# Kernel tuning notes

Measured on AMD Instinct MI355X. Metric: run time of the kernel, lower is better.

Reference implementation:

```python
import jax, jax.numpy as jnp
import numpy as np

T, B, I, H, L = 512, 32, 512, 1024, 2


def setup_inputs() -> dict:
    key = jax.random.key(0)
    ks = jax.random.split(key, 10)
    std = 1.0 / np.sqrt(H)
    u = lambda k, shape: jax.random.uniform(k, shape, jnp.float32, -std, std)
    return {
        "x": jax.random.normal(ks[0], (T, B, I), jnp.float32),
        "Wxh0": u(ks[1], (4 * H, I)),
        "bxh0": u(ks[2], (4 * H,)),
        "Whh0": u(ks[3], (4 * H, H)),
        "bhh0": u(ks[4], (4 * H,)),
        "Wxh1": u(ks[5], (4 * H, H)),
        "bxh1": u(ks[6], (4 * H,)),
        "Whh1": u(ks[7], (4 * H, H)),
        "bhh1": u(ks[8], (4 * H,)),
    }


def _lstm_layer(x_seq, Wxh, bxh, Whh, bhh):
    # x_seq: (T, B, D_in). Precompute input projections for all timesteps.
    xg = jnp.einsum('tbi,gi->tbg', x_seq, Wxh) + bxh  # (T, B, 4H)
    h0 = jnp.zeros((x_seq.shape[1], H), x_seq.dtype)
    c0 = jnp.zeros_like(h0)

    def step(carry, xg_t):
        h, c = carry
        gates = xg_t + h @ Whh.T + bhh  # (B, 4H)
        i_g, f_g, g_g, o_g = jnp.split(gates, 4, axis=-1)
        c_new = jax.nn.sigmoid(f_g) * c + jax.nn.sigmoid(i_g) * jnp.tanh(g_g)
        h_new = jax.nn.sigmoid(o_g) * jnp.tanh(c_new)
        return (h_new, c_new), h_new

    (h_T, c_T), hs = jax.lax.scan(step, (h0, c0), xg)
    return hs, h_T, c_T  # hs: (T, B, H)


def reference(x, Wxh0, bxh0, Whh0, bhh0, Wxh1, bxh1, Whh1, bhh1):
    # Layer 0 consumes raw input; layer 1 consumes layer-0 hidden sequence.
    # Processing layer-by-layer is mathematically identical to the original
    # interleaved (t, layer) loop for a stacked unidirectional LSTM.
    hs0, h0T, c0T = _lstm_layer(x, Wxh0, bxh0, Whh0, bhh0)
    hs1, h1T, c1T = _lstm_layer(hs0, Wxh1, bxh1, Whh1, bhh1)
    output = hs1  # (T, B, H): hidden of last layer at each timestep
    h_n = jnp.stack([h0T, h1T])  # (L, B, H)
    c_n = jnp.stack([c0T, c1T])
    return output, h_n, c_n
```

## Files before the change

### kernel.cpp

```cpp
#include <hip/hip_runtime.h>


typedef unsigned short u16;
typedef __attribute__((ext_vector_type(8))) __bf16 bf16x8;
typedef __attribute__((ext_vector_type(8))) u16 u16x8;
typedef __attribute__((ext_vector_type(4))) float f32x4;
typedef __attribute__((ext_vector_type(2))) float f32x2;
typedef __attribute__((ext_vector_type(4))) int i32x4;
typedef __attribute__((ext_vector_type(4))) unsigned int u32x4;

#define HN_OFF 16777216
#define CN_OFF 16842752

__device__ __forceinline__ u16 f2bf(float f) {
  unsigned u = __builtin_bit_cast(unsigned, f);
  u += 0x7FFFu + ((u >> 16) & 1u);
  return (u16)(u >> 16);
}
__device__ __forceinline__ float sgm(float x) { return 1.f / (1.f + __expf(-x)); }
__device__ __forceinline__ float tnh(float x) { return 2.f / (1.f + __expf(-2.f * x)) - 1.f; }

__device__ __forceinline__ bf16x8 ld16(const u16* p) {
  u32x4 v = *reinterpret_cast<const u32x4*>(p);
  return __builtin_bit_cast(bf16x8, v);
}
__device__ __forceinline__ bf16x8 lds16(const char* p) {
  u32x4 v = *reinterpret_cast<const u32x4*>(p);
  return __builtin_bit_cast(bf16x8, v);
}
__device__ __forceinline__ f32x4 mfma16(bf16x8 a, bf16x8 b, f32x4 c) {
  return __builtin_amdgcn_mfma_f32_16x16x32_bf16(a, b, c, 0, 0, 0);
}

__device__ __forceinline__ void poll_flags(const int* f, int lane, int s) {
  const int* p0 = f + (lane << 2);
  const int* p1 = f + 256 + (lane << 2);
  for (;;) {
    i32x4 a, b;
    asm volatile("global_load_dwordx4 %0, %2, off sc0 sc1\n\t"
                 "global_load_dwordx4 %1, %3, off sc0 sc1\n\t"
                 "s_waitcnt vmcnt(0)"
                 : "=v"(a), "=v"(b) : "v"(p0), "v"(p1) : "memory");
    if (__all((a[0] >= s) & (a[1] >= s) & (a[2] >= s) & (a[3] >= s) &
              (b[0] >= s) & (b[1] >= s) & (b[2] >= s) & (b[3] >= s))) break;
  }
}
__device__ __forceinline__ void poll_epoch(const int* ep, int s) {
  for (;;) {
    int e;
    asm volatile("global_load_dword %0, %1, off sc0 sc1\n\ts_waitcnt vmcnt(0)"
                 : "=v"(e) : "v"(ep) : "memory");
    if (e >= s) break;
  }
}

template <int C0, int C1>
__device__ __forceinline__ void chunks_h0(const u16* __restrict__ A,
                                          const char* w0, const char* w1, int lane,
                                          f32x4& p0, f32x4& p1, f32x4& q0, f32x4& q1) {
  const int r = lane & 15, kq = (lane >> 4) * 8, swz = (r & 7) << 4;
#pragma unroll
  for (int c = C0; c < C1; ++c) {
    const u16* ap = A + r * 1024 + c * 32 + kq;
    bf16x8 a0 = ld16(ap);
    bf16x8 a1 = ld16(ap + 16 * 1024);
    bf16x8 b0 = lds16(w0 + r * 3072 + ((c * 64 + kq * 2) ^ swz));
    bf16x8 b1 = lds16(w1 + r * 4096 + (((c + 32) * 64 + kq * 2) ^ swz));
    p0 = mfma16(a0, b0, p0);  p1 = mfma16(a1, b0, p1);
    q0 = mfma16(a0, b1, q0);  q1 = mfma16(a1, b1, q1);
  }
}
template <int C0, int C1>
__device__ __forceinline__ void chunks_h1(const u16* __restrict__ A,
                                          const char* w1, int lane,
                                          f32x4& p0, f32x4& p1) {
  const int r = lane & 15, kq = (lane >> 4) * 8, swz = (r & 7) << 4;
#pragma unroll
  for (int c = C0; c < C1; ++c) {
    const u16* ap = A + r * 1024 + c * 32 + kq;
    bf16x8 a0 = ld16(ap);
    bf16x8 a1 = ld16(ap + 16 * 1024);
    bf16x8 bw = lds16(w1 + r * 4096 + ((c * 64 + kq * 2) ^ swz));
    p0 = mfma16(a0, bw, p0);  p1 = mfma16(a1, bw, p1);
  }
}
template <int C0, int C1>
__device__ __forceinline__ void chunks_x(const u16* __restrict__ A,
                                         const char* w0, int lane,
                                         f32x4& q0, f32x4& q1) {
  const int r = lane & 15, kq = (lane >> 4) * 8, swz = (r & 7) << 4;
#pragma unroll
  for (int c = C0; c < C1; ++c) {
    const u16* ap = A + r * 512 + c * 32 + kq;
    bf16x8 a0 = ld16(ap);
    bf16x8 a1 = ld16(ap + 16 * 512);
    bf16x8 bw = lds16(w0 + r * 3072 + (((c + 32) * 64 + kq * 2) ^ swz));
    q0 = mfma16(a0, bw, q0);  q1 = mfma16(a1, bw, q1);
  }
}

__global__ __launch_bounds__(512, 2) void lstm_fused(
    const u16* __restrict__ xbf,
    const float* __restrict__ Whh0, const float* __restrict__ Wxh0,
    const float* __restrict__ Whh1, const float* __restrict__ Wxh1,
    const float* __restrict__ bxh0, const float* __restrict__ bhh0,
    const float* __restrict__ bxh1, const float* __restrict__ bhh1,
    u16* __restrict__ h0seq, u16* __restrict__ h1seq,
    int* __restrict__ flagbase,
    float* __restrict__ out) {
  extern __shared__ char smem[];
  const char* w0 = smem;
  const char* w1 = smem + 49152;
  auto part = reinterpret_cast<float(*)[32][18]>(smem + 114688);
  float* bias0 = reinterpret_cast<float*>(smem + 151552);
  float* bias1 = reinterpret_cast<float*>(smem + 151616);
  volatile int* go = reinterpret_cast<volatile int*>(smem + 151680);

  int* flag0 = flagbase;
  int* flag1 = flagbase + 256;
  int* epoch = flagbase + 512;

  const int tid = threadIdx.x;
  const int wg = blockIdx.x;
  const int wid = tid >> 6, lane = tid & 63;

  if (tid == 0) go[0] = 0;
  for (int g = tid; g < 3072; g += 512) {
    int n = g / 192, gi = g % 192, kc = gi * 8;
    int gr = ((n >> 2) << 10) + (wg << 2) + (n & 3);
    const float* src = (kc < 1024) ? (Whh0 + gr * 1024 + kc) : (Wxh0 + gr * 512 + (kc - 1024));
    f32x4 lo = *reinterpret_cast<const f32x4*>(src);
    f32x4 hi = *reinterpret_cast<const f32x4*>(src + 4);
    u16x8 o;
    o[0]=f2bf(lo[0]); o[1]=f2bf(lo[1]); o[2]=f2bf(lo[2]); o[3]=f2bf(lo[3]);
    o[4]=f2bf(hi[0]); o[5]=f2bf(hi[1]); o[6]=f2bf(hi[2]); o[7]=f2bf(hi[3]);
    *reinterpret_cast<u16x8*>(smem + n * 3072 + ((gi * 16) ^ ((n & 7) << 4))) = o;
  }
  for (int g = tid; g < 4096; g += 512) {
    int n = g / 256, gi = g % 256, kc = gi * 8;
    int gr = ((n >> 2) << 10) + (wg << 2) + (n & 3);
    const float* src = (kc < 1024) ? (Whh1 + gr * 1024 + kc) : (Wxh1 + gr * 1024 + (kc - 1024));
    f32x4 lo = *reinterpret_cast<const f32x4*>(src);
    f32x4 hi = *reinterpret_cast<const f32x4*>(src + 4);
    u16x8 o;
    o[0]=f2bf(lo[0]); o[1]=f2bf(lo[1]); o[2]=f2bf(lo[2]); o[3]=f2bf(lo[3]);
    o[4]=f2bf(hi[0]); o[5]=f2bf(hi[1]); o[6]=f2bf(hi[2]); o[7]=f2bf(hi[3]);
    *reinterpret_cast<u16x8*>(smem + 49152 + n * 4096 + ((gi * 16) ^ ((n & 7) << 4))) = o;
  }
  if (tid < 16) {
    int gr = ((tid >> 2) << 10) + (wg << 2) + (tid & 3);
    bias0[tid] = bxh0[gr] + bhh0[gr];
    bias1[tid] = bxh1[gr] + bhh1[gr];
  }
  __syncthreads();

  float c0a = 0.f, c0b = 0.f, c1a = 0.f, c1b = 0.f;
  const int bg = lane >> 1, jjb = (lane & 1) << 1;
  const int colb = (wg << 2) + jjb;

  for (int s = 0; s <= 512; ++s) {
    const u16* h0slot = h0seq + s * 32768;
    const u16* h1prev = h1seq + (s - 1) * 32768;
    f32x4 p0 = {0,0,0,0}, p1 = {0,0,0,0}, q0 = {0,0,0,0}, q1 = {0,0,0,0};

    if (wid >= 4 && s < 512) {
      const u16* xbt = xbf + s * 16384;
      if      (wid == 4) chunks_x<0,  4 >(xbt, w0, lane, q0, q1);
      else if (wid == 5) chunks_x<4,  8 >(xbt, w0, lane, q0, q1);
      else if (wid == 6) chunks_x<8,  12>(xbt, w0, lane, q0, q1);
      else               chunks_x<12, 16>(xbt, w0, lane, q0, q1);
    }

    if (s >= 1) {
      if (wid == 0) {
        if (wg == 0) {
          poll_flags(flag0, lane, s);
          if (lane == 0) {
            int sv = s;
            asm volatile("global_store_dword %0, %1, off sc0 sc1"
                         :: "v"(epoch), "v"(sv) : "memory");
          }
        } else {
          poll_epoch(epoch, s);
        }
        if (lane == 0) go[0] = s;
      } else {
        while (go[0] < s) __builtin_amdgcn_s_sleep(1);
      }
    }

    if (wid < 4) {
      if      (wid == 0) chunks_h0<0,  8 >(h0slot, w0, w1, lane, p0, p1, q0, q1);
      else if (wid == 1) chunks_h0<8,  16>(h0slot, w0, w1, lane, p0, p1, q0, q1);
      else if (wid == 2) chunks_h0<16, 24>(h0slot, w0, w1, lane, p0, p1, q0, q1);
      else               chunks_h0<24, 32>(h0slot, w0, w1, lane, p0, p1, q0, q1);
    } else if (s >= 1) {
      if      (wid == 4) chunks_h1<0,  8 >(h1prev, w1, lane, p0, p1);
      else if (wid == 5) chunks_h1<8,  16>(h1prev, w1, lane, p0, p1);
      else if (wid == 6) chunks_h1<16, 24>(h1prev, w1, lane, p0, p1);
      else               chunks_h1<24, 32>(h1prev, w1, lane, p0, p1);
    }

    {
      const int n = lane & 15, br = (lane >> 4) * 4;
#pragma unroll
      for (int j = 0; j < 4; ++j) {
        part[wid][br + j][n]          = p0[j];
        part[wid][br + j + 16][n]     = p1[j];
        part[8 + wid][br + j][n]      = q0[j];
        part[8 + wid][br + j + 16][n] = q1[j];
      }
    }
    __syncthreads();

    if (wid == 1) {
      if (s < 512) {
        float v[4][2];
#pragma unroll
        for (int gi = 0; gi < 4; ++gi) {
          const int n = (gi << 2) + jjb;
          float s0 = bias0[n], s1 = bias0[n + 1];
#pragma unroll
          for (int p = 0; p < 4; ++p) {
            f32x2 a = *reinterpret_cast<const f32x2*>(&part[p][bg][n]);
            f32x2 b = *reinterpret_cast<const f32x2*>(&part[12 + p][bg][n]);
            s0 += a[0] + b[0];  s1 += a[1] + b[1];
          }
          v[gi][0] = s0; v[gi][1] = s1;
        }
        c0a = sgm(v[1][0]) * c0a + sgm(v[0][0]) * tnh(v[2][0]);
        c0b = sgm(v[1][1]) * c0b + sgm(v[0][1]) * tnh(v[2][1]);
        const float ha = sgm(v[3][0]) * tnh(c0a), hb = sgm(v[3][1]) * tnh(c0b);
        unsigned pk = (unsigned)f2bf(ha) | ((unsigned)f2bf(hb) << 16);
        u16* hp = h0seq + (s + 1) * 32768 + bg * 1024 + colb;
        asm volatile("global_store_dword %0, %1, off sc0 sc1" :: "v"(hp), "v"(pk) : "memory");
        asm volatile("s_waitcnt vmcnt(0)" ::: "memory");
        if (lane == 0) {
          int* fp = flag0 + wg;  int fv = s + 1;
          asm volatile("global_store_dword %0, %1, off sc0 sc1" :: "v"(fp), "v"(fv) : "memory");
        }
        if (s == 511) {
          *reinterpret_cast<f32x2*>(out + HN_OFF + bg * 1024 + colb) = f32x2{ha, hb};
          *reinterpret_cast<f32x2*>(out + CN_OFF + bg * 1024 + colb) = f32x2{c0a, c0b};
        }
      }
    } else if (wid == 5) {
      if (s >= 1) {
        float v[4][2];
#pragma unroll
        for (int gi = 0; gi < 4; ++gi) {
          const int n = (gi << 2) + jjb;
          float s0 = bias1[n], s1 = bias1[n + 1];
#pragma unroll
          for (int p = 4; p < 12; ++p) {
            f32x2 a = *reinterpret_cast<const f32x2*>(&part[p][bg][n]);
            s0 += a[0];  s1 += a[1];
          }
          v[gi][0] = s0; v[gi][1] = s1;
        }
        c1a = sgm(v[1][0]) * c1a + sgm(v[0][0]) * tnh(v[2][0]);
        c1b = sgm(v[1][1]) * c1b + sgm(v[0][1]) * tnh(v[2][1]);
        const float ha = sgm(v[3][0]) * tnh(c1a), hb = sgm(v[3][1]) * tnh(c1b);
        unsigned pk = (unsigned)f2bf(ha) | ((unsigned)f2bf(hb) << 16);
        u16* hp = h1seq + s * 32768 + bg * 1024 + colb;
        asm volatile("global_store_dword %0, %1, off sc0 sc1" :: "v"(hp), "v"(pk) : "memory");
        asm volatile("s_waitcnt vmcnt(0)" ::: "memory");
        if (lane == 0) {
          int* fp = flag1 + wg;  int fv = s + 1;
          asm volatile("global_store_dword %0, %1, off sc0 sc1" :: "v"(fp), "v"(fv) : "memory");
        }
        const int t1 = s - 1;
        *reinterpret_cast<f32x2*>(out + t1 * 32768 + bg * 1024 + colb) = f32x2{ha, hb};
        if (t1 == 511) {
          *reinterpret_cast<f32x2*>(out + HN_OFF + 32768 + bg * 1024 + colb) = f32x2{ha, hb};
          *reinterpret_cast<f32x2*>(out + CN_OFF + 32768 + bg * 1024 + colb) = f32x2{c1a, c1b};
        }
      } else if (lane == 0) {
        int* fp = flag1 + wg;  int fv = 1;
        asm volatile("global_store_dword %0, %1, off sc0 sc1" :: "v"(fp), "v"(fv) : "memory");
      }
    }
  }
}

__global__ void cvt_bf16(const float* __restrict__ s, u16* __restrict__ d, int n) {
  int i = (blockIdx.x * blockDim.x + threadIdx.x) * 4;
  const int stride = gridDim.x * blockDim.x * 4;
  typedef __attribute__((ext_vector_type(4))) u16 u16x4;
  for (; i < n; i += stride) {
    f32x4 v = *reinterpret_cast<const f32x4*>(s + i);
    u16x4 o;
    o[0] = f2bf(v[0]); o[1] = f2bf(v[1]); o[2] = f2bf(v[2]); o[3] = f2bf(v[3]);
    *reinterpret_cast<u16x4*>(d + i) = o;
  }
}

extern "C" void kernel_launch(void* const* d_in, const int* in_sizes, int n_in,
                              void* d_out, int out_size, void* d_ws, size_t ws_size,
                              hipStream_t stream) {
  const float* x    = (const float*)d_in[0];
  const float* Wxh0 = (const float*)d_in[1];
  const float* bxh0 = (const float*)d_in[2];
  const float* Whh0 = (const float*)d_in[3];
  const float* bhh0 = (const float*)d_in[4];
  const float* Wxh1 = (const float*)d_in[5];
  const float* bxh1 = (const float*)d_in[6];
  const float* Whh1 = (const float*)d_in[7];
  const float* bhh1 = (const float*)d_in[8];
  char* ws = (char*)d_ws;
  u16* xbf      = (u16*)(ws);
  u16* h0seq    = (u16*)(ws + 16777216);
  u16* h1seq    = (u16*)(ws + 50397184);
  int* flagbase = (int*)(ws + 84017152);

  cvt_bf16<<<2048, 256, 0, stream>>>(x, xbf, 512 * 32 * 512);
  (void)hipMemsetAsync(h0seq, 0, 65536, stream);
  (void)hipMemsetAsync(h1seq, 0, 65536, stream);
  (void)hipMemsetAsync(flagbase, 0, 4096, stream);

  (void)hipFuncSetAttribute(reinterpret_cast<const void*>(lstm_fused),
                            hipFuncAttributeMaxDynamicSharedMemorySize, 151744);
  lstm_fused<<<dim3(256), dim3(512), 151744, stream>>>(
      xbf, Whh0, Wxh0, Whh1, Wxh1, bxh0, bhh0, bxh1, bhh1,
      h0seq, h1seq, flagbase, (float*)d_out);
}
```

Before: 3.517 ms.

## Poll per-block flags directly in every workgroup and batch A-operand loads

Removes the two-hop barrier in which block 0 polled all flags and then published an epoch that the other blocks polled. Every workgroup now polls the flag array itself, cutting one global round-trip of latency from each timestep. The matmul chunk helpers also issue all global A-operand loads before the MFMA loop so their latencies overlap. This raises register pressure and puts more polling traffic on the shared flag lines.

```diff
diff --git a/kernel.cpp b/kernel.cpp
--- a/kernel.cpp
+++ b/kernel.cpp
@@ -45,29 +45,27 @@
               (b[0] >= s) & (b[1] >= s) & (b[2] >= s) & (b[3] >= s))) break;
   }
 }
-__device__ __forceinline__ void poll_epoch(const int* ep, int s) {
-  for (;;) {
-    int e;
-    asm volatile("global_load_dword %0, %1, off sc0 sc1\n\ts_waitcnt vmcnt(0)"
-                 : "=v"(e) : "v"(ep) : "memory");
-    if (e >= s) break;
-  }
-}
 
 template <int C0, int C1>
 __device__ __forceinline__ void chunks_h0(const u16* __restrict__ A,
                                           const char* w0, const char* w1, int lane,
                                           f32x4& p0, f32x4& p1, f32x4& q0, f32x4& q1) {
   const int r = lane & 15, kq = (lane >> 4) * 8, swz = (r & 7) << 4;
-#pragma unroll
-  for (int c = C0; c < C1; ++c) {
-    const u16* ap = A + r * 1024 + c * 32 + kq;
-    bf16x8 a0 = ld16(ap);
-    bf16x8 a1 = ld16(ap + 16 * 1024);
+  constexpr int N = C1 - C0;
+  bf16x8 A0[N], A1[N];
+#pragma unroll
+  for (int i = 0; i < N; ++i) {
+    const u16* ap = A + r * 1024 + (C0 + i) * 32 + kq;
+    A0[i] = ld16(ap);
+    A1[i] = ld16(ap + 16 * 1024);
+  }
+#pragma unroll
+  for (int i = 0; i < N; ++i) {
+    const int c = C0 + i;
     bf16x8 b0 = lds16(w0 + r * 3072 + ((c * 64 + kq * 2) ^ swz));
     bf16x8 b1 = lds16(w1 + r * 4096 + (((c + 32) * 64 + kq * 2) ^ swz));
-    p0 = mfma16(a0, b0, p0);  p1 = mfma16(a1, b0, p1);
-    q0 = mfma16(a0, b1, q0);  q1 = mfma16(a1, b1, q1);
+    p0 = mfma16(A0[i], b0, p0);  p1 = mfma16(A1[i], b0, p1);
+    q0 = mfma16(A0[i], b1, q0);  q1 = mfma16(A1[i], b1, q1);
   }
 }
 template <int C0, int C1>
@@ -75,13 +73,19 @@
                                           const char* w1, int lane,
                                           f32x4& p0, f32x4& p1) {
   const int r = lane & 15, kq = (lane >> 4) * 8, swz = (r & 7) << 4;
-#pragma unroll
-  for (int c = C0; c < C1; ++c) {
-    const u16* ap = A + r * 1024 + c * 32 + kq;
-    bf16x8 a0 = ld16(ap);
-    bf16x8 a1 = ld16(ap + 16 * 1024);
+  constexpr int N = C1 - C0;
+  bf16x8 A0[N], A1[N];
+#pragma unroll
+  for (int i = 0; i < N; ++i) {
+    const u16* ap = A + r * 1024 + (C0 + i) * 32 + kq;
+    A0[i] = ld16(ap);
+    A1[i] = ld16(ap + 16 * 1024);
+  }
+#pragma unroll
+  for (int i = 0; i < N; ++i) {
+    const int c = C0 + i;
     bf16x8 bw = lds16(w1 + r * 4096 + ((c * 64 + kq * 2) ^ swz));
-    p0 = mfma16(a0, bw, p0);  p1 = mfma16(a1, bw, p1);
+    p0 = mfma16(A0[i], bw, p0);  p1 = mfma16(A1[i], bw, p1);
   }
 }
 template <int C0, int C1>
@@ -89,13 +93,19 @@
                                          const char* w0, int lane,
                                          f32x4& q0, f32x4& q1) {
   const int r = lane & 15, kq = (lane >> 4) * 8, swz = (r & 7) << 4;
-#pragma unroll
-  for (int c = C0; c < C1; ++c) {
-    const u16* ap = A + r * 512 + c * 32 + kq;
-    bf16x8 a0 = ld16(ap);
-    bf16x8 a1 = ld16(ap + 16 * 512);
+  constexpr int N = C1 - C0;
+  bf16x8 A0[N], A1[N];
+#pragma unroll
+  for (int i = 0; i < N; ++i) {
+    const u16* ap = A + r * 512 + (C0 + i) * 32 + kq;
+    A0[i] = ld16(ap);
+    A1[i] = ld16(ap + 16 * 512);
+  }
+#pragma unroll
+  for (int i = 0; i < N; ++i) {
+    const int c = C0 + i;
     bf16x8 bw = lds16(w0 + r * 3072 + (((c + 32) * 64 + kq * 2) ^ swz));
-    q0 = mfma16(a0, bw, q0);  q1 = mfma16(a1, bw, q1);
+    q0 = mfma16(A0[i], bw, q0);  q1 = mfma16(A1[i], bw, q1);
   }
 }
 
@@ -118,7 +128,6 @@
 
   int* flag0 = flagbase;
   int* flag1 = flagbase + 256;
-  int* epoch = flagbase + 512;
 
   const int tid = threadIdx.x;
   const int wg = blockIdx.x;
@@ -173,16 +182,7 @@
 
     if (s >= 1) {
       if (wid == 0) {
-        if (wg == 0) {
-          poll_flags(flag0, lane, s);
-          if (lane == 0) {
-            int sv = s;
-            asm volatile("global_store_dword %0, %1, off sc0 sc1"
-                         :: "v"(epoch), "v"(sv) : "memory");
-          }
-        } else {
-          poll_epoch(epoch, s);
-        }
+        poll_flags(flagbase, lane, s);
         if (lane == 0) go[0] = s;
       } else {
         while (go[0] < s) __builtin_amdgcn_s_sleep(1);
@@ -316,7 +316,7 @@
   cvt_bf16<<<2048, 256, 0, stream>>>(x, xbf, 512 * 32 * 512);
   (void)hipMemsetAsync(h0seq, 0, 65536, stream);
   (void)hipMemsetAsync(h1seq, 0, 65536, stream);
-  (void)hipMemsetAsync(flagbase, 0, 4096, stream);
+  (void)hipMemsetAsync(flagbase, 0, 2048, stream);
 
   (void)hipFuncSetAttribute(reinterpret_cast<const void*>(lstm_fused),
                             hipFuncAttributeMaxDynamicSharedMemorySize, 151744);
```

After: 5.691 ms. +61.8%, slower.

## Replace centralized epoch barrier with replicated flags and sentinel-polled hidden loads

Applied to the files above, without the earlier changes.

Removes the two-level barrier (block 0 polls all flags, then broadcasts an epoch) and replaces it with flag arrays replicated eight times. Each block polls its own replica, and producers write the flag without first waiting for their data stores to complete. Hidden-state buffers are pre-filled with a 0xFF sentinel so consumers spin on the actual h data until it is valid, which tolerates flags arriving before data. The weight LDS layout also changes from a swizzled layout to a fragment-contiguous one. The cost is extra memsets of the whole sequence buffers, and correctness now depends on no real bf16 pair equalling the sentinel.

```diff
diff --git a/kernel.cpp b/kernel.cpp
--- a/kernel.cpp
+++ b/kernel.cpp
@@ -11,6 +11,7 @@
 
 #define HN_OFF 16777216
 #define CN_OFF 16842752
+#define SENT 0xFFFFFFFFu
 
 __device__ __forceinline__ u16 f2bf(float f) {
   unsigned u = __builtin_bit_cast(unsigned, f);
@@ -20,10 +21,6 @@
 __device__ __forceinline__ float sgm(float x) { return 1.f / (1.f + __expf(-x)); }
 __device__ __forceinline__ float tnh(float x) { return 2.f / (1.f + __expf(-2.f * x)) - 1.f; }
 
-__device__ __forceinline__ bf16x8 ld16(const u16* p) {
-  u32x4 v = *reinterpret_cast<const u32x4*>(p);
-  return __builtin_bit_cast(bf16x8, v);
-}
 __device__ __forceinline__ bf16x8 lds16(const char* p) {
   u32x4 v = *reinterpret_cast<const u32x4*>(p);
   return __builtin_bit_cast(bf16x8, v);
@@ -32,70 +29,77 @@
   return __builtin_amdgcn_mfma_f32_16x16x32_bf16(a, b, c, 0, 0, 0);
 }
 
-__device__ __forceinline__ void poll_flags(const int* f, int lane, int s) {
-  const int* p0 = f + (lane << 2);
-  const int* p1 = f + 256 + (lane << 2);
+__device__ __forceinline__ void ld_h_pair(const u16* ap, bf16x8& a0, bf16x8& a1) {
+  u32x4 ua = *reinterpret_cast<const u32x4*>(ap);
+  u32x4 ub = *reinterpret_cast<const u32x4*>(ap + 16 * 1024);
+  while (__any((ua[0] == SENT) | (ua[1] == SENT) | (ua[2] == SENT) | (ua[3] == SENT) |
+               (ub[0] == SENT) | (ub[1] == SENT) | (ub[2] == SENT) | (ub[3] == SENT))) {
+    asm volatile("global_load_dwordx4 %0, %2, off sc0 sc1\n\t"
+                 "global_load_dwordx4 %1, %3, off sc0 sc1\n\t"
+                 "s_waitcnt vmcnt(0)"
+                 : "=v"(ua), "=v"(ub) : "v"(ap), "v"(ap + 16 * 1024) : "memory");
+  }
+  a0 = __builtin_bit_cast(bf16x8, ua);
+  a1 = __builtin_bit_cast(bf16x8, ub);
+}
+
+template <int C0, int C1>
+__device__ __forceinline__ void chunks_h0(const u16* __restrict__ A,
+                                          const char* w0f, const char* w1f, int lane,
+                                          f32x4& p0, f32x4& p1, f32x4& q0, f32x4& q1) {
+  const int r = lane & 15, kq = (lane >> 4) * 8, lo = lane << 4;
+#pragma unroll
+  for (int c = C0; c < C1; ++c) {
+    bf16x8 a0, a1;
+    ld_h_pair(A + r * 1024 + c * 32 + kq, a0, a1);
+    bf16x8 b0 = lds16(w0f + (c << 10) + lo);
+    bf16x8 b1 = lds16(w1f + ((c + 32) << 10) + lo);
+    p0 = mfma16(a0, b0, p0);  p1 = mfma16(a1, b0, p1);
+    q0 = mfma16(a0, b1, q0);  q1 = mfma16(a1, b1, q1);
+  }
+}
+template <int C0, int C1>
+__device__ __forceinline__ void chunks_h1(const u16* __restrict__ A,
+                                          const char* w1f, int lane,
+                                          f32x4& p0, f32x4& p1) {
+  const int r = lane & 15, kq = (lane >> 4) * 8, lo = lane << 4;
+#pragma unroll
+  for (int c = C0; c < C1; ++c) {
+    bf16x8 a0, a1;
+    ld_h_pair(A + r * 1024 + c * 32 + kq, a0, a1);
+    bf16x8 bw = lds16(w1f + (c << 10) + lo);
+    p0 = mfma16(a0, bw, p0);  p1 = mfma16(a1, bw, p1);
+  }
+}
+template <int C0, int C1>
+__device__ __forceinline__ void chunks_x(const u16* __restrict__ A,
+                                         const char* w0f, int lane,
+                                         f32x4& q0, f32x4& q1) {
+  const int r = lane & 15, kq = (lane >> 4) * 8, lo = lane << 4;
+#pragma unroll
+  for (int c = C0; c < C1; ++c) {
+    const u16* ap = A + r * 512 + c * 32 + kq;
+    u32x4 va = *reinterpret_cast<const u32x4*>(ap);
+    u32x4 vb = *reinterpret_cast<const u32x4*>(ap + 16 * 512);
+    bf16x8 a0 = __builtin_bit_cast(bf16x8, va);
+    bf16x8 a1 = __builtin_bit_cast(bf16x8, vb);
+    bf16x8 bw = lds16(w0f + ((c + 32) << 10) + lo);
+    q0 = mfma16(a0, bw, q0);  q1 = mfma16(a1, bw, q1);
+  }
+}
+
+__device__ __forceinline__ void poll_rep(const int* rep, int lane, int s) {
+  const int* pa = rep + (lane << 2);
+  const int* pb = rep + 256 + (lane << 2);
   for (;;) {
     i32x4 a, b;
     asm volatile("global_load_dwordx4 %0, %2, off sc0 sc1\n\t"
                  "global_load_dwordx4 %1, %3, off sc0 sc1\n\t"
                  "s_waitcnt vmcnt(0)"
-                 : "=v"(a), "=v"(b) : "v"(p0), "v"(p1) : "memory");
+                 : "=v"(a), "=v"(b) : "v"(pa), "v"(pb) : "memory");
     if (__all((a[0] >= s) & (a[1] >= s) & (a[2] >= s) & (a[3] >= s) &
               (b[0] >= s) & (b[1] >= s) & (b[2] >= s) & (b[3] >= s))) break;
-  }
-}
-__device__ __forceinline__ void poll_epoch(const int* ep, int s) {
-  for (;;) {
-    int e;
-    asm volatile("global_load_dword %0, %1, off sc0 sc1\n\ts_waitcnt vmcnt(0)"
-                 : "=v"(e) : "v"(ep) : "memory");
-    if (e >= s) break;
-  }
-}
-
-template <int C0, int C1>
-__device__ __forceinline__ void chunks_h0(const u16* __restrict__ A,
-                                          const char* w0, const char* w1, int lane,
-                                          f32x4& p0, f32x4& p1, f32x4& q0, f32x4& q1) {
-  const int r = lane & 15, kq = (lane >> 4) * 8, swz = (r & 7) << 4;
-#pragma unroll
-  for (int c = C0; c < C1; ++c) {
-    const u16* ap = A + r * 1024 + c * 32 + kq;
-    bf16x8 a0 = ld16(ap);
-    bf16x8 a1 = ld16(ap + 16 * 1024);
-    bf16x8 b0 = lds16(w0 + r * 3072 + ((c * 64 + kq * 2) ^ swz));
-    bf16x8 b1 = lds16(w1 + r * 4096 + (((c + 32) * 64 + kq * 2) ^ swz));
-    p0 = mfma16(a0, b0, p0);  p1 = mfma16(a1, b0, p1);
-    q0 = mfma16(a0, b1, q0);  q1 = mfma16(a1, b1, q1);
-  }
-}
-template <int C0, int C1>
-__device__ __forceinline__ void chunks_h1(const u16* __restrict__ A,
-                                          const char* w1, int lane,
-                                          f32x4& p0, f32x4& p1) {
-  const int r = lane & 15, kq = (lane >> 4) * 8, swz = (r & 7) << 4;
-#pragma unroll
-  for (int c = C0; c < C1; ++c) {
-    const u16* ap = A + r * 1024 + c * 32 + kq;
-    bf16x8 a0 = ld16(ap);
-    bf16x8 a1 = ld16(ap + 16 * 1024);
-    bf16x8 bw = lds16(w1 + r * 4096 + ((c * 64 + kq * 2) ^ swz));
-    p0 = mfma16(a0, bw, p0);  p1 = mfma16(a1, bw, p1);
-  }
-}
-template <int C0, int C1>
-__device__ __forceinline__ void chunks_x(const u16* __restrict__ A,
-                                         const char* w0, int lane,
-                                         f32x4& q0, f32x4& q1) {
-  const int r = lane & 15, kq = (lane >> 4) * 8, swz = (r & 7) << 4;
-#pragma unroll
-  for (int c = C0; c < C1; ++c) {
-    const u16* ap = A + r * 512 + c * 32 + kq;
-    bf16x8 a0 = ld16(ap);
-    bf16x8 a1 = ld16(ap + 16 * 512);
-    bf16x8 bw = lds16(w0 + r * 3072 + (((c + 32) * 64 + kq * 2) ^ swz));
-    q0 = mfma16(a0, bw, q0);  q1 = mfma16(a1, bw, q1);
+    __builtin_amdgcn_s_sleep(1);
   }
 }
 
@@ -109,43 +113,39 @@
     int* __restrict__ flagbase,
     float* __restrict__ out) {
   extern __shared__ char smem[];
-  const char* w0 = smem;
-  const char* w1 = smem + 49152;
-  auto part = reinterpret_cast<float(*)[32][18]>(smem + 114688);
-  float* bias0 = reinterpret_cast<float*>(smem + 151552);
-  float* bias1 = reinterpret_cast<float*>(smem + 151616);
-  volatile int* go = reinterpret_cast<volatile int*>(smem + 151680);
-
-  int* flag0 = flagbase;
-  int* flag1 = flagbase + 256;
-  int* epoch = flagbase + 512;
+  const char* w0f = smem;
+  const char* w1f = smem + 49152;
+  auto part = reinterpret_cast<float(*)[32][16]>(smem + 114688);
+  float* bias0 = reinterpret_cast<float*>(smem + 147456);
+  float* bias1 = reinterpret_cast<float*>(smem + 147520);
 
   const int tid = threadIdx.x;
   const int wg = blockIdx.x;
   const int wid = tid >> 6, lane = tid & 63;
 
-  if (tid == 0) go[0] = 0;
   for (int g = tid; g < 3072; g += 512) {
-    int n = g / 192, gi = g % 192, kc = gi * 8;
+    int c = g >> 6, l = g & 63, n = l & 15;
+    int kb = c * 32 + ((l >> 4) << 3);
     int gr = ((n >> 2) << 10) + (wg << 2) + (n & 3);
-    const float* src = (kc < 1024) ? (Whh0 + gr * 1024 + kc) : (Wxh0 + gr * 512 + (kc - 1024));
+    const float* src = (kb < 1024) ? (Whh0 + gr * 1024 + kb) : (Wxh0 + gr * 512 + (kb - 1024));
     f32x4 lo = *reinterpret_cast<const f32x4*>(src);
     f32x4 hi = *reinterpret_cast<const f32x4*>(src + 4);
     u16x8 o;
     o[0]=f2bf(lo[0]); o[1]=f2bf(lo[1]); o[2]=f2bf(lo[2]); o[3]=f2bf(lo[3]);
     o[4]=f2bf(hi[0]); o[5]=f2bf(hi[1]); o[6]=f2bf(hi[2]); o[7]=f2bf(hi[3]);
-    *reinterpret_cast<u16x8*>(smem + n * 3072 + ((gi * 16) ^ ((n & 7) << 4))) = o;
+    *reinterpret_cast<u16x8*>(smem + (c << 10) + (l << 4)) = o;
   }
   for (int g = tid; g < 4096; g += 512) {
-    int n = g / 256, gi = g % 256, kc = gi * 8;
+    int c = g >> 6, l = g & 63, n = l & 15;
+    int kb = c * 32 + ((l >> 4) << 3);
     int gr = ((n >> 2) << 10) + (wg << 2) + (n & 3);
-    const float* src = (kc < 1024) ? (Whh1 + gr * 1024 + kc) : (Wxh1 + gr * 1024 + (kc - 1024));
+    const float* src = (kb < 1024) ? (Whh1 + gr * 1024 + kb) : (Wxh1 + gr * 1024 + (kb - 1024));
     f32x4 lo = *reinterpret_cast<const f32x4*>(src);
     f32x4 hi = *reinterpret_cast<const f32x4*>(src + 4);
     u16x8 o;
     o[0]=f2bf(lo[0]); o[1]=f2bf(lo[1]); o[2]=f2bf(lo[2]); o[3]=f2bf(lo[3]);
     o[4]=f2bf(hi[0]); o[5]=f2bf(hi[1]); o[6]=f2bf(hi[2]); o[7]=f2bf(hi[3]);
-    *reinterpret_cast<u16x8*>(smem + 49152 + n * 4096 + ((gi * 16) ^ ((n & 7) << 4))) = o;
+    *reinterpret_cast<u16x8*>(smem + 49152 + (c << 10) + (l << 4)) = o;
   }
   if (tid < 16) {
     int gr = ((tid >> 2) << 10) + (wg << 2) + (tid & 3);
@@ -157,6 +157,7 @@
   float c0a = 0.f, c0b = 0.f, c1a = 0.f, c1b = 0.f;
   const int bg = lane >> 1, jjb = (lane & 1) << 1;
   const int colb = (wg << 2) + jjb;
+  const int* rep = flagbase + ((wg & 7) << 9);
 
   for (int s = 0; s <= 512; ++s) {
     const u16* h0slot = h0seq + s * 32768;
@@ -165,40 +166,24 @@
 
     if (wid >= 4 && s < 512) {
       const u16* xbt = xbf + s * 16384;
-      if      (wid == 4) chunks_x<0,  4 >(xbt, w0, lane, q0, q1);
-      else if (wid == 5) chunks_x<4,  8 >(xbt, w0, lane, q0, q1);
-      else if (wid == 6) chunks_x<8,  12>(xbt, w0, lane, q0, q1);
-      else               chunks_x<12, 16>(xbt, w0, lane, q0, q1);
+      if      (wid == 4) chunks_x<0,  4 >(xbt, w0f, lane, q0, q1);
+      else if (wid == 5) chunks_x<4,  8 >(xbt, w0f, lane, q0, q1);
+      else if (wid == 6) chunks_x<8,  12>(xbt, w0f, lane, q0, q1);
+      else               chunks_x<12, 16>(xbt, w0f, lane, q0, q1);
     }
-
-    if (s >= 1) {
-      if (wid == 0) {
-        if (wg == 0) {
-          poll_flags(flag0, lane, s);
-          if (lane == 0) {
-            int sv = s;
-            asm volatile("global_store_dword %0, %1, off sc0 sc1"
-                         :: "v"(epoch), "v"(sv) : "memory");
-          }
-        } else {
-          poll_epoch(epoch, s);
-        }
-        if (lane == 0) go[0] = s;
-      } else {
-        while (go[0] < s) __builtin_amdgcn_s_sleep(1);
-      }
-    }
+    if (wid == 0 && s >= 1) poll_rep(rep, lane, s);
+    __syncthreads();
 
     if (wid < 4) {
-      if      (wid == 0) chunks_h0<0,  8 >(h0slot, w0, w1, lane, p0, p1, q0, q1);
-      else if (wid == 1) chunks_h0<8,  16>(h0slot, w0, w1, lane, p0, p1, q0, q1);
-      else if (wid == 2) chunks_h0<16, 24>(h0slot, w0, w1, lane, p0, p1, q0, q1);
-      else               chunks_h0<24, 32>(h0slot, w0, w1, lane, p0, p1, q0, q1);
+      if      (wid == 0) chunks_h0<0,  8 >(h0slot, w0f, w1f, lane, p0, p1, q0, q1);
+      else if (wid == 1) chunks_h0<8,  16>(h0slot, w0f, w1f, lane, p0, p1, q0, q1);
+      else if (wid == 2) chunks_h0<16, 24>(h0slot, w0f, w1f, lane, p0, p1, q0, q1);
+      else               chunks_h0<24, 32>(h0slot, w0f, w1f, lane, p0, p1, q0, q1);
     } else if (s >= 1) {
-      if      (wid == 4) chunks_h1<0,  8 >(h1prev, w1, lane, p0, p1);
-      else if (wid == 5) chunks_h1<8,  16>(h1prev, w1, lane, p0, p1);
-      else if (wid == 6) chunks_h1<16, 24>(h1prev, w1, lane, p0, p1);
-      else               chunks_h1<24, 32>(h1prev, w1, lane, p0, p1);
+      if      (wid == 4) chunks_h1<0,  8 >(h1prev, w1f, lane, p0, p1);
+      else if (wid == 5) chunks_h1<8,  16>(h1prev, w1f, lane, p0, p1);
+      else if (wid == 6) chunks_h1<16, 24>(h1prev, w1f, lane, p0, p1);
+      else               chunks_h1<24, 32>(h1prev, w1f, lane, p0, p1);
     }
 
     {
@@ -234,9 +219,8 @@
         unsigned pk = (unsigned)f2bf(ha) | ((unsigned)f2bf(hb) << 16);
         u16* hp = h0seq + (s + 1) * 32768 + bg * 1024 + colb;
         asm volatile("global_store_dword %0, %1, off sc0 sc1" :: "v"(hp), "v"(pk) : "memory");
-        asm volatile("s_waitcnt vmcnt(0)" ::: "memory");
-        if (lane == 0) {
-          int* fp = flag0 + wg;  int fv = s + 1;
+        if (lane < 8) {
+          int* fp = flagbase + (lane << 9) + wg;  int fv = s + 1;
           asm volatile("global_store_dword %0, %1, off sc0 sc1" :: "v"(fp), "v"(fv) : "memory");
         }
         if (s == 511) {
@@ -264,9 +248,8 @@
         unsigned pk = (unsigned)f2bf(ha) | ((unsigned)f2bf(hb) << 16);
         u16* hp = h1seq + s * 32768 + bg * 1024 + colb;
         asm volatile("global_store_dword %0, %1, off sc0 sc1" :: "v"(hp), "v"(pk) : "memory");
-        asm volatile("s_waitcnt vmcnt(0)" ::: "memory");
-        if (lane == 0) {
-          int* fp = flag1 + wg;  int fv = s + 1;
+        if (lane < 8) {
+          int* fp = flagbase + (lane << 9) + 256 + wg;  int fv = s + 1;
           asm volatile("global_store_dword %0, %1, off sc0 sc1" :: "v"(fp), "v"(fv) : "memory");
         }
         const int t1 = s - 1;
@@ -275,8 +258,8 @@
           *reinterpret_cast<f32x2*>(out + HN_OFF + 32768 + bg * 1024 + colb) = f32x2{ha, hb};
           *reinterpret_cast<f32x2*>(out + CN_OFF + 32768 + bg * 1024 + colb) = f32x2{c1a, c1b};
         }
-      } else if (lane == 0) {
-        int* fp = flag1 + wg;  int fv = 1;
+      } else if (lane < 8) {
+        int* fp = flagbase + (lane << 9) + 256 + wg;  int fv = 1;
         asm volatile("global_store_dword %0, %1, off sc0 sc1" :: "v"(fp), "v"(fv) : "memory");
       }
     }
@@ -314,13 +297,15 @@
   int* flagbase = (int*)(ws + 84017152);
 
   cvt_bf16<<<2048, 256, 0, stream>>>(x, xbf, 512 * 32 * 512);
+  (void)hipMemsetAsync(h0seq, 0xFF, 513 * 65536, stream);
+  (void)hipMemsetAsync(h1seq, 0xFF, 513 * 65536, stream);
   (void)hipMemsetAsync(h0seq, 0, 65536, stream);
   (void)hipMemsetAsync(h1seq, 0, 65536, stream);
-  (void)hipMemsetAsync(flagbase, 0, 4096, stream);
+  (void)hipMemsetAsync(flagbase, 0, 16384, stream);
 
   (void)hipFuncSetAttribute(reinterpret_cast<const void*>(lstm_fused),
-                            hipFuncAttributeMaxDynamicSharedMemorySize, 151744);
-  lstm_fused<<<dim3(256), dim3(512), 151744, stream>>>(
+                            hipFuncAttributeMaxDynamicSharedMemorySize, 147584);
+  lstm_fused<<<dim3(256), dim3(512), 147584, stream>>>(
       xbf, Whh0, Wxh0, Whh1, Wxh1, bxh0, bhh0, bxh1, bhh1,
       h0seq, h1seq, flagbase, (float*)d_out);
 }
```

Result: slower. 4.464 ms (+26.9%).
